# Performance work log

Hardware: AMD Instinct MI355X
Metric: run time of the kernel (lower is better)

## Reference

```python
import jax, jax.numpy as jnp
import numpy as np

DIM = 256
N_EMBED = 8192
DECAY = 0.99
EPS = 1e-05


def setup_inputs() -> dict:
    key = jax.random.key(0)
    k1, k2, k3, k4 = jax.random.split(key, 4)
    z = jax.random.normal(k1, (16, 32, 32, DIM), dtype=jnp.float32)
    embedding = jax.random.normal(k2, (DIM, N_EMBED), dtype=jnp.float32)
    cluster_size = jax.random.uniform(k3, (N_EMBED,), dtype=jnp.float32)
    embedding_avg = jax.random.normal(k4, (DIM, N_EMBED), dtype=jnp.float32)
    return {"z": z, "embedding": embedding, "cluster_size": cluster_size,
            "embedding_avg": embedding_avg}


def reference(z, embedding, cluster_size, embedding_avg):
    flatten = z.reshape(-1, DIM)  # [N, dim]
    dist = ((flatten ** 2).sum(1, keepdims=True)
            - 2.0 * flatten @ embedding
            + (embedding ** 2).sum(0, keepdims=True))
    embed_ind_flat = jnp.argmin(dist, axis=1)  # [N] int
    embed_ind = embed_ind_flat.reshape(z.shape[:-1])
    # Gather codes: embedding is [dim, n_embed]; quantize [..., dim]
    quantize = jnp.take(embedding.T, embed_ind_flat, axis=0).reshape(z.shape)

    # EMA codebook update (training path), via segment sums (no dense one-hot)
    onehot_sum = jax.ops.segment_sum(
        jnp.ones_like(embed_ind_flat, dtype=flatten.dtype),
        embed_ind_flat, num_segments=N_EMBED)  # [n_embed]
    embed_sum = jax.ops.segment_sum(flatten, embed_ind_flat,
                                    num_segments=N_EMBED).T  # [dim, n_embed]
    new_cluster_size = cluster_size * DECAY + (1.0 - DECAY) * onehot_sum
    new_embedding_avg = embedding_avg * DECAY + (1.0 - DECAY) * embed_sum
    n = new_cluster_size.sum()
    smoothed = (new_cluster_size + EPS) / (n + N_EMBED * EPS) * n
    new_embedding = new_embedding_avg / smoothed[None, :]

    diff = jnp.mean((jax.lax.stop_gradient(quantize) - z) ** 2)
    quantize_st = z + jax.lax.stop_gradient(quantize - z)
    return (quantize_st, diff, embed_ind, new_embedding,
            new_cluster_size, new_embedding_avg)
```

## Files before the change

kernel.cpp:

```cpp
#include <hip/hip_runtime.h>


#define DIMC  256
#define NEMB  8192
#define NROWS 16384

#define OUT_Q      0u
#define OUT_DIFF   4194304u
#define OUT_IDX    4194305u
#define OUT_NEWEMB 4210689u
#define OUT_NEWCS  6307841u
#define OUT_NEWAVG 6316033u

#define WS_EHI    0u
#define WS_ELO    1048576u
#define WS_COUNT  2097152u
#define WS_DIFF   2105344u
#define WS_N      2105345u
#define WS_ENORM  2105346u
#define WS_PACK   2113540u

typedef __attribute__((ext_vector_type(8))) short short8;
typedef __attribute__((ext_vector_type(4))) float f32x4;

__device__ inline void split_bf16(float x, unsigned short& h, unsigned short& l) {
  unsigned u = __float_as_uint(x);
  unsigned r = u + 0x7FFFu + ((u >> 16) & 1u);
  h = (unsigned short)(r >> 16);
  float hf = __uint_as_float((unsigned)h << 16);
  float lo = x - hf;
  unsigned u2 = __float_as_uint(lo);
  unsigned r2 = u2 + 0x7FFFu + ((u2 >> 16) & 1u);
  l = (unsigned short)(r2 >> 16);
}

__device__ inline float bf16_f(unsigned short u) {
  return __uint_as_float((unsigned)u << 16);
}

__global__ __launch_bounds__(256) void prep_kernel(
    const float* __restrict__ z, const float* __restrict__ emb,
    unsigned short* __restrict__ z_hi, unsigned short* __restrict__ z_lo,
    unsigned short* __restrict__ e_hi, unsigned short* __restrict__ e_lo,
    float* __restrict__ enorm, float* __restrict__ embsum) {
  const int b = blockIdx.x;
  const int t = threadIdx.x;
  __shared__ float tile[64][68];
  __shared__ float red[4][64];

  if (b < 1024) {
#pragma unroll
    for (int it = 0; it < 4; ++it) {
      const int idx = (b * 256 + t) + it * 262144;
      const float4 v = reinterpret_cast<const float4*>(z)[idx];
      ushort4 h, l;
      split_bf16(v.x, h.x, l.x);
      split_bf16(v.y, h.y, l.y);
      split_bf16(v.z, h.z, l.z);
      split_bf16(v.w, h.w, l.w);
      reinterpret_cast<ushort4*>(z_hi)[idx] = h;
      reinterpret_cast<ushort4*>(z_lo)[idx] = l;
    }
  } else if (b < 1536) {
    const int bb = b - 1024;
    const int n0 = (bb & 127) * 64;
    const int k0 = (bb >> 7) * 64;
    const int c4 = (t & 15) * 4;
    const int rr = t >> 4;
#pragma unroll
    for (int i = 0; i < 4; ++i) {
      const int kl = rr + i * 16;
      const float4 v = *reinterpret_cast<const float4*>(
          &emb[(size_t)(k0 + kl) * NEMB + n0 + c4]);
      *reinterpret_cast<float4*>(&tile[kl][c4]) = v;
    }
    __syncthreads();
#pragma unroll
    for (int i = 0; i < 4; ++i) {
      const int nr = rr + i * 16;
      float4 v;
      v.x = tile[c4 + 0][nr];
      v.y = tile[c4 + 1][nr];
      v.z = tile[c4 + 2][nr];
      v.w = tile[c4 + 3][nr];
      const size_t off = (size_t)(n0 + nr) * DIMC + k0 + c4;
      ushort4 h, l;
      split_bf16(v.x, h.x, l.x);
      split_bf16(v.y, h.y, l.y);
      split_bf16(v.z, h.z, l.z);
      split_bf16(v.w, h.w, l.w);
      *reinterpret_cast<ushort4*>(&e_hi[off]) = h;
      *reinterpret_cast<ushort4*>(&e_lo[off]) = l;
    }
  } else if (b < 2048) {
    const int bb = b - 1536;
    const float4 zero = {0.f, 0.f, 0.f, 0.f};
#pragma unroll
    for (int it = 0; it < 4; ++it)
      reinterpret_cast<float4*>(embsum)[bb * 1024 + t + it * 256] = zero;
  } else {
    const int l = t & 63;
    const int dg = t >> 6;
    const int e = (b - 2048) * 64 + l;
    float s = 0.f;
#pragma unroll 8
    for (int d = dg * 64; d < dg * 64 + 64; ++d) {
      const float v = emb[(size_t)d * NEMB + e];
      s = fmaf(v, v, s);
    }
    red[dg][l] = s;
    __syncthreads();
    if (dg == 0) enorm[e] = red[0][l] + red[1][l] + red[2][l] + red[3][l];
  }
}

__global__ __launch_bounds__(256, 2) void argmin_mfma_kernel(
    const unsigned short* __restrict__ z_hi, const unsigned short* __restrict__ z_lo,
    const unsigned short* __restrict__ e_hi, const unsigned short* __restrict__ e_lo,
    const float* __restrict__ enorm, unsigned long long* __restrict__ pack) {
  __shared__ short za[16384];
  __shared__ short eb[16384];
  const int tid = threadIdx.x;
  const int bid = blockIdx.x;
  const int r0 = (bid >> 2) * 128;
  const int ebase = (bid & 3) * 2048;
  const int tx = tid & 15;
  const int q = (tid >> 4) & 3;
  const int wave = tid >> 6;
  const int wm = wave & 1;
  const int wn = wave >> 1;

  float rmin[4][4];
  int ridx[4][4];
#pragma unroll
  for (int i = 0; i < 4; ++i)
#pragma unroll
    for (int r = 0; r < 4; ++r) { rmin[i][r] = 3.4028235e38f; ridx[i][r] = 0; }

  for (int nt = 0; nt < 16; ++nt) {
    const int n0 = ebase + nt * 128;
    f32x4 acc[4][4];
#pragma unroll
    for (int i = 0; i < 4; ++i)
#pragma unroll
      for (int j = 0; j < 4; ++j) acc[i][j] = (f32x4)0.0f;

    for (int kt = 0; kt < 4; ++kt) {
      const int k0 = kt * 64;
      __syncthreads();
#pragma unroll
      for (int it = 0; it < 8; ++it) {
        const int P = tid + it * 256;
        const int row = P >> 4;
        const int p = P & 15;
        const int o = (p & 7) ^ (row & 7);
        const unsigned short* zsrc =
            ((p & 8) ? z_lo : z_hi) + (size_t)(r0 + row) * DIMC + k0 + o * 8;
        __builtin_amdgcn_global_load_lds(
            (const __attribute__((address_space(1))) unsigned int*)zsrc,
            (__attribute__((address_space(3))) unsigned int*)&za[P * 8], 16, 0, 0);
        const unsigned short* esrc =
            ((p & 8) ? e_lo : e_hi) + (size_t)(n0 + row) * DIMC + k0 + o * 8;
        __builtin_amdgcn_global_load_lds(
            (const __attribute__((address_space(1))) unsigned int*)esrc,
            (__attribute__((address_space(3))) unsigned int*)&eb[P * 8], 16, 0, 0);
      }
      __syncthreads();
#pragma unroll
      for (int ks = 0; ks < 2; ++ks) {
        short8 ah[4], al[4], bh[4], bl[4];
#pragma unroll
        for (int i = 0; i < 4; ++i) {
          const int rl = wm * 64 + i * 16 + tx;
          const int oa = (ks * 4 + q) ^ (rl & 7);
          ah[i] = *reinterpret_cast<const short8*>(&za[rl * 128 + oa * 8]);
          al[i] = *reinterpret_cast<const short8*>(&za[rl * 128 + (oa + 8) * 8]);
          const int cl = wn * 64 + i * 16 + tx;
          const int ob = (ks * 4 + q) ^ (cl & 7);
          bh[i] = *reinterpret_cast<const short8*>(&eb[cl * 128 + ob * 8]);
          bl[i] = *reinterpret_cast<const short8*>(&eb[cl * 128 + (ob + 8) * 8]);
        }
#pragma unroll
        for (int i = 0; i < 4; ++i)
#pragma unroll
          for (int j = 0; j < 4; ++j) {
            acc[i][j] = __builtin_amdgcn_mfma_f32_16x16x32_bf16(ah[i], bh[j],
                                                               acc[i][j], 0, 0, 0);
            acc[i][j] = __builtin_amdgcn_mfma_f32_16x16x32_bf16(ah[i], bl[j],
                                                               acc[i][j], 0, 0, 0);
            acc[i][j] = __builtin_amdgcn_mfma_f32_16x16x32_bf16(al[i], bh[j],
                                                               acc[i][j], 0, 0, 0);
          }
      }
    }
#pragma unroll
    for (int j = 0; j < 4; ++j) {
      const int col = n0 + wn * 64 + j * 16 + tx;
      const float en = enorm[col];
#pragma unroll
      for (int i = 0; i < 4; ++i)
#pragma unroll
        for (int r = 0; r < 4; ++r) {
          const float s = en - 2.0f * acc[i][j][r];
          if (s < rmin[i][r]) { rmin[i][r] = s; ridx[i][r] = col; }
        }
    }
  }
#pragma unroll
  for (int i = 0; i < 4; ++i)
#pragma unroll
    for (int r = 0; r < 4; ++r) {
      float v = rmin[i][r];
      int ix = ridx[i][r];
#pragma unroll
      for (int off = 1; off < 16; off <<= 1) {
        const float ov = __shfl_xor(v, off, 16);
        const int oi = __shfl_xor(ix, off, 16);
        if (ov < v || (ov == v && oi < ix)) { v = ov; ix = oi; }
      }
      if (tx == 0) {
        const unsigned int fb = __float_as_uint(v);
        const unsigned int sb = (fb & 0x80000000u) ? ~fb : (fb | 0x80000000u);
        const unsigned long long key =
            ((unsigned long long)sb << 13) | (unsigned long long)(unsigned)ix;
        atomicMin(&pack[r0 + wm * 64 + i * 16 + q * 4 + r], key);
      }
    }
}

__global__ __launch_bounds__(256) void gather_update_kernel(
    const float* __restrict__ z, const unsigned short* __restrict__ e_hi,
    const unsigned short* __restrict__ e_lo,
    const unsigned long long* __restrict__ pack, float* __restrict__ out_q,
    float* __restrict__ out_idx, float* __restrict__ embsum,
    float* __restrict__ count, float* __restrict__ diff_acc) {
  const int row = blockIdx.x * 4 + (threadIdx.x >> 6);
  const int lane = threadIdx.x & 63;
  const int e = (int)(pack[row] & 8191ULL);
  if (lane == 0) out_idx[row] = (float)e;
  const float4 zv =
      *reinterpret_cast<const float4*>(&z[(size_t)row * DIMC + lane * 4]);
  const ushort4 h =
      *reinterpret_cast<const ushort4*>(&e_hi[(size_t)e * DIMC + lane * 4]);
  const ushort4 l =
      *reinterpret_cast<const ushort4*>(&e_lo[(size_t)e * DIMC + lane * 4]);
  const float q0 = bf16_f(h.x) + bf16_f(l.x);
  const float q1 = bf16_f(h.y) + bf16_f(l.y);
  const float q2 = bf16_f(h.z) + bf16_f(l.z);
  const float q3 = bf16_f(h.w) + bf16_f(l.w);
  const float d0 = q0 - zv.x, d1 = q1 - zv.y, d2 = q2 - zv.z, d3 = q3 - zv.w;
  float4 st;
  st.x = zv.x + d0; st.y = zv.y + d1; st.z = zv.z + d2; st.w = zv.w + d3;
  *reinterpret_cast<float4*>(&out_q[(size_t)row * DIMC + lane * 4]) = st;

  atomicAdd(&embsum[(size_t)e * DIMC + lane * 4 + 0], zv.x);
  atomicAdd(&embsum[(size_t)e * DIMC + lane * 4 + 1], zv.y);
  atomicAdd(&embsum[(size_t)e * DIMC + lane * 4 + 2], zv.z);
  atomicAdd(&embsum[(size_t)e * DIMC + lane * 4 + 3], zv.w);

  float local = d0 * d0 + d1 * d1 + d2 * d2 + d3 * d3;
#pragma unroll
  for (int off = 32; off > 0; off >>= 1) local += __shfl_down(local, off, 64);

  __shared__ float dred[4];
  if (lane == 0) {
    dred[threadIdx.x >> 6] = local;
    atomicAdd(&count[e], 1.0f);
  }
  __syncthreads();
  if (threadIdx.x == 0)
    atomicAdd(diff_acc, dred[0] + dred[1] + dred[2] + dred[3]);
}

__global__ __launch_bounds__(256) void fin_a_kernel(
    const float* __restrict__ eavg, const float* __restrict__ embsum,
    float* __restrict__ avgtmp, const float* __restrict__ cs,
    const float* __restrict__ count, float* __restrict__ out_ncs,
    float* __restrict__ out_diff, const float* __restrict__ diff_acc,
    float* __restrict__ n_acc) {
  const int b = blockIdx.x;
  const int t = threadIdx.x;
  __shared__ float tile[64][68];
  if (b < 512) {
    const int e0 = (b & 127) * 64;
    const int d0 = (b >> 7) * 64;
    const int c4 = (t & 15) * 4;
    const int rr = t >> 4;
#pragma unroll
    for (int i = 0; i < 4; ++i) {
      const int er = rr + i * 16;
      const float4 v = *reinterpret_cast<const float4*>(
          &embsum[(size_t)(e0 + er) * DIMC + d0 + c4]);
      *reinterpret_cast<float4*>(&tile[er][c4]) = v;
    }
    __syncthreads();
#pragma unroll
    for (int i = 0; i < 4; ++i) {
      const int dr = rr + i * 16;
      const size_t g = (size_t)(d0 + dr) * NEMB + e0 + c4;
      const float4 av = *reinterpret_cast<const float4*>(&eavg[g]);
      float4 o;
      o.x = av.x * 0.99f + 0.01f * tile[c4 + 0][dr];
      o.y = av.y * 0.99f + 0.01f * tile[c4 + 1][dr];
      o.z = av.z * 0.99f + 0.01f * tile[c4 + 2][dr];
      o.w = av.w * 0.99f + 0.01f * tile[c4 + 3][dr];
      *reinterpret_cast<float4*>(&avgtmp[g]) = o;
    }
  } else {
    const int g = (b - 512) * 256 + t;
    const float ncs = cs[g] * 0.99f + 0.01f * count[g];
    out_ncs[g] = ncs;
    float s = ncs;
#pragma unroll
    for (int off = 32; off > 0; off >>= 1) s += __shfl_down(s, off, 64);
    __shared__ float red[4];
    if ((t & 63) == 0) red[t >> 6] = s;
    __syncthreads();
    if (t == 0) atomicAdd(n_acc, red[0] + red[1] + red[2] + red[3]);
    if (g == 0) out_diff[0] = diff_acc[0] * (1.0f / 4194304.0f);
  }
}

__global__ __launch_bounds__(256) void fin2_kernel(
    const float* __restrict__ ncs_out, const float* __restrict__ n_acc,
    float* __restrict__ out_avg, float* __restrict__ out_emb_and_avgtmp) {
  const int g = blockIdx.x * 256 + threadIdx.x;
  const int e = g & 8191;
  const float avg = out_emb_and_avgtmp[g];
  const float n = n_acc[0];
  const float ncs = ncs_out[e];
  const float smoothed = (ncs + 1e-5f) / (n + (float)NEMB * 1e-5f) * n;
  out_avg[g] = avg;
  out_emb_and_avgtmp[g] = avg / smoothed;
}

extern "C" void kernel_launch(void* const* d_in, const int* in_sizes, int n_in,
                              void* d_out, int out_size, void* d_ws,
                              size_t ws_size, hipStream_t stream) {
  const float* z = (const float*)d_in[0];
  const float* emb = (const float*)d_in[1];
  const float* cs = (const float*)d_in[2];
  const float* eavg = (const float*)d_in[3];
  float* out = (float*)d_out;
  float* ws = (float*)d_ws;

  unsigned short* e_hi = (unsigned short*)(ws + WS_EHI);
  unsigned short* e_lo = (unsigned short*)(ws + WS_ELO);
  float* ws_count = ws + WS_COUNT;
  float* ws_diff = ws + WS_DIFF;
  float* ws_n = ws + WS_N;
  float* ws_enorm = ws + WS_ENORM;
  unsigned long long* ws_pack = (unsigned long long*)(ws + WS_PACK);

  unsigned short* z_hi = (unsigned short*)(out + OUT_Q);
  unsigned short* z_lo = (unsigned short*)(out + OUT_Q + 2097152);
  float* embsum = out + OUT_NEWAVG;
  float* avgtmp = out + OUT_NEWEMB;

  hipMemsetAsync(ws_count, 0, (size_t)8194 * sizeof(float), stream);
  hipMemsetAsync(ws_pack, 0xFF, (size_t)NROWS * sizeof(unsigned long long),
                 stream);

  prep_kernel<<<2176, 256, 0, stream>>>(z, emb, z_hi, z_lo, e_hi, e_lo,
                                        ws_enorm, embsum);
  argmin_mfma_kernel<<<512, 256, 0, stream>>>(z_hi, z_lo, e_hi, e_lo, ws_enorm,
                                              ws_pack);
  gather_update_kernel<<<NROWS / 4, 256, 0, stream>>>(
      z, e_hi, e_lo, ws_pack, out + OUT_Q, out + OUT_IDX, embsum, ws_count,
      ws_diff);
  fin_a_kernel<<<544, 256, 0, stream>>>(eavg, embsum, avgtmp, cs, ws_count,
                                        out + OUT_NEWCS, out + OUT_DIFF,
                                        ws_diff, ws_n);
  fin2_kernel<<<(DIMC * NEMB) / 256, 256, 0, stream>>>(
      out + OUT_NEWCS, ws_n, out + OUT_NEWAVG, avgtmp);
}
```

Before: 396.0 us.

## Precompute cluster-size total analytically and fold memsets into prep kernel

The sum of new cluster sizes is computed up front as 0.99*sum(cs) + 0.01*N, because the one-hot counts always total the row count. This lets the first finalize kernel write the normalized embedding directly and drops the atomic reduction. The final kernel recovers the EMA average by multiplying the stored embedding by the smoothed size, and the two hipMemsetAsync calls are replaced by extra blocks in the prep kernel. The risk is small floating-point mismatch, since the average is reconstructed through a divide followed by a multiply instead of being stored exactly.

```diff
diff --git a/kernel.cpp b/kernel.cpp
--- a/kernel.cpp
+++ b/kernel.cpp
@@ -40,9 +40,11 @@
 
 __global__ __launch_bounds__(256) void prep_kernel(
     const float* __restrict__ z, const float* __restrict__ emb,
-    unsigned short* __restrict__ z_hi, unsigned short* __restrict__ z_lo,
-    unsigned short* __restrict__ e_hi, unsigned short* __restrict__ e_lo,
-    float* __restrict__ enorm, float* __restrict__ embsum) {
+    const float* __restrict__ cs, unsigned short* __restrict__ z_hi,
+    unsigned short* __restrict__ z_lo, unsigned short* __restrict__ e_hi,
+    unsigned short* __restrict__ e_lo, float* __restrict__ enorm,
+    float* __restrict__ embsum, unsigned long long* __restrict__ pack,
+    float* __restrict__ count_diff, float* __restrict__ n_out) {
   const int b = blockIdx.x;
   const int t = threadIdx.x;
   __shared__ float tile[64][68];
@@ -98,7 +100,7 @@
 #pragma unroll
     for (int it = 0; it < 4; ++it)
       reinterpret_cast<float4*>(embsum)[bb * 1024 + t + it * 256] = zero;
-  } else {
+  } else if (b < 2176) {
     const int l = t & 63;
     const int dg = t >> 6;
     const int e = (b - 2048) * 64 + l;
@@ -111,6 +113,25 @@
     red[dg][l] = s;
     __syncthreads();
     if (dg == 0) enorm[e] = red[0][l] + red[1][l] + red[2][l] + red[3][l];
+  } else if (b < 2184) {
+    const int bb = b - 2176;
+    const uint4 ff = {~0u, ~0u, ~0u, ~0u};
+#pragma unroll
+    for (int it = 0; it < 4; ++it)
+      reinterpret_cast<uint4*>(pack)[bb * 1024 + t + it * 256] = ff;
+  } else if (b == 2184) {
+    for (int i = t; i < 8193; i += 256) count_diff[i] = 0.f;
+  } else {
+    float s = 0.f;
+#pragma unroll
+    for (int i = 0; i < 32; ++i) s += cs[t + i * 256];
+#pragma unroll
+    for (int off = 32; off > 0; off >>= 1) s += __shfl_down(s, off, 64);
+    if ((t & 63) == 0) red[0][t >> 6] = s;
+    __syncthreads();
+    if (t == 0)
+      n_out[0] = 0.99f * (red[0][0] + red[0][1] + red[0][2] + red[0][3]) +
+                 163.84f;
   }
 }
 
@@ -272,20 +293,27 @@
     atomicAdd(diff_acc, dred[0] + dred[1] + dred[2] + dred[3]);
 }
 
-__global__ __launch_bounds__(256) void fin_a_kernel(
+__global__ __launch_bounds__(256) void fin1_kernel(
     const float* __restrict__ eavg, const float* __restrict__ embsum,
-    float* __restrict__ avgtmp, const float* __restrict__ cs,
-    const float* __restrict__ count, float* __restrict__ out_ncs,
-    float* __restrict__ out_diff, const float* __restrict__ diff_acc,
-    float* __restrict__ n_acc) {
+    const float* __restrict__ cs, const float* __restrict__ count,
+    const float* __restrict__ n_ptr, const float* __restrict__ diff_acc,
+    float* __restrict__ out_emb, float* __restrict__ out_ncs,
+    float* __restrict__ out_diff) {
   const int b = blockIdx.x;
   const int t = threadIdx.x;
   __shared__ float tile[64][68];
+  __shared__ float rs[64];
   if (b < 512) {
     const int e0 = (b & 127) * 64;
     const int d0 = (b >> 7) * 64;
     const int c4 = (t & 15) * 4;
     const int rr = t >> 4;
+    if (t < 64) {
+      const float n = n_ptr[0];
+      const float ncs = cs[e0 + t] * 0.99f + 0.01f * count[e0 + t];
+      const float sm = (ncs + 1e-5f) / (n + 0.08192f) * n;
+      rs[t] = 1.0f / sm;
+    }
 #pragma unroll
     for (int i = 0; i < 4; ++i) {
       const int er = rr + i * 16;
@@ -300,38 +328,29 @@
       const size_t g = (size_t)(d0 + dr) * NEMB + e0 + c4;
       const float4 av = *reinterpret_cast<const float4*>(&eavg[g]);
       float4 o;
-      o.x = av.x * 0.99f + 0.01f * tile[c4 + 0][dr];
-      o.y = av.y * 0.99f + 0.01f * tile[c4 + 1][dr];
-      o.z = av.z * 0.99f + 0.01f * tile[c4 + 2][dr];
-      o.w = av.w * 0.99f + 0.01f * tile[c4 + 3][dr];
-      *reinterpret_cast<float4*>(&avgtmp[g]) = o;
+      o.x = (av.x * 0.99f + 0.01f * tile[c4 + 0][dr]) * rs[c4 + 0];
+      o.y = (av.y * 0.99f + 0.01f * tile[c4 + 1][dr]) * rs[c4 + 1];
+      o.z = (av.z * 0.99f + 0.01f * tile[c4 + 2][dr]) * rs[c4 + 2];
+      o.w = (av.w * 0.99f + 0.01f * tile[c4 + 3][dr]) * rs[c4 + 3];
+      *reinterpret_cast<float4*>(&out_emb[g]) = o;
     }
   } else {
     const int g = (b - 512) * 256 + t;
-    const float ncs = cs[g] * 0.99f + 0.01f * count[g];
-    out_ncs[g] = ncs;
-    float s = ncs;
-#pragma unroll
-    for (int off = 32; off > 0; off >>= 1) s += __shfl_down(s, off, 64);
-    __shared__ float red[4];
-    if ((t & 63) == 0) red[t >> 6] = s;
-    __syncthreads();
-    if (t == 0) atomicAdd(n_acc, red[0] + red[1] + red[2] + red[3]);
+    out_ncs[g] = cs[g] * 0.99f + 0.01f * count[g];
     if (g == 0) out_diff[0] = diff_acc[0] * (1.0f / 4194304.0f);
   }
 }
 
-__global__ __launch_bounds__(256) void fin2_kernel(
-    const float* __restrict__ ncs_out, const float* __restrict__ n_acc,
-    float* __restrict__ out_avg, float* __restrict__ out_emb_and_avgtmp) {
+__global__ __launch_bounds__(256) void fin2b_kernel(
+    const float* __restrict__ cs, const float* __restrict__ count,
+    const float* __restrict__ n_ptr, const float* __restrict__ out_emb,
+    float* __restrict__ out_avg) {
   const int g = blockIdx.x * 256 + threadIdx.x;
   const int e = g & 8191;
-  const float avg = out_emb_and_avgtmp[g];
-  const float n = n_acc[0];
-  const float ncs = ncs_out[e];
-  const float smoothed = (ncs + 1e-5f) / (n + (float)NEMB * 1e-5f) * n;
-  out_avg[g] = avg;
-  out_emb_and_avgtmp[g] = avg / smoothed;
+  const float n = n_ptr[0];
+  const float ncs = cs[e] * 0.99f + 0.01f * count[e];
+  const float sm = (ncs + 1e-5f) / (n + 0.08192f) * n;
+  out_avg[g] = out_emb[g] * sm;
 }
 
 extern "C" void kernel_launch(void* const* d_in, const int* in_sizes, int n_in,
@@ -355,22 +374,18 @@
   unsigned short* z_hi = (unsigned short*)(out + OUT_Q);
   unsigned short* z_lo = (unsigned short*)(out + OUT_Q + 2097152);
   float* embsum = out + OUT_NEWAVG;
-  float* avgtmp = out + OUT_NEWEMB;
-
-  hipMemsetAsync(ws_count, 0, (size_t)8194 * sizeof(float), stream);
-  hipMemsetAsync(ws_pack, 0xFF, (size_t)NROWS * sizeof(unsigned long long),
-                 stream);
-
-  prep_kernel<<<2176, 256, 0, stream>>>(z, emb, z_hi, z_lo, e_hi, e_lo,
-                                        ws_enorm, embsum);
+
+  prep_kernel<<<2186, 256, 0, stream>>>(z, emb, cs, z_hi, z_lo, e_hi, e_lo,
+                                        ws_enorm, embsum, ws_pack, ws_count,
+                                        ws_n);
   argmin_mfma_kernel<<<512, 256, 0, stream>>>(z_hi, z_lo, e_hi, e_lo, ws_enorm,
                                               ws_pack);
   gather_update_kernel<<<NROWS / 4, 256, 0, stream>>>(
       z, e_hi, e_lo, ws_pack, out + OUT_Q, out + OUT_IDX, embsum, ws_count,
       ws_diff);
-  fin_a_kernel<<<544, 256, 0, stream>>>(eavg, embsum, avgtmp, cs, ws_count,
-                                        out + OUT_NEWCS, out + OUT_DIFF,
-                                        ws_diff, ws_n);
-  fin2_kernel<<<(DIMC * NEMB) / 256, 256, 0, stream>>>(
-      out + OUT_NEWCS, ws_n, out + OUT_NEWAVG, avgtmp);
-}
+  fin1_kernel<<<544, 256, 0, stream>>>(eavg, embsum, cs, ws_count, ws_n,
+                                       ws_diff, out + OUT_NEWEMB,
+                                       out + OUT_NEWCS, out + OUT_DIFF);
+  fin2b_kernel<<<(DIMC * NEMB) / 256, 256, 0, stream>>>(
+      cs, ws_count, ws_n, out + OUT_NEWEMB, out + OUT_NEWAVG);
+}
```

Result: no change. 390.0 us (-1.5%).
